# Optimization experiments

Measured on AMD Instinct MI355X. Metric: run time of the kernel, lower is better.

The kernel has to match this reference:

```python
import jax, jax.numpy as jnp
import numpy as np

B, F_NODES, E = 1024, 128, 1024   # graphs, nodes/graph, edges/graph
H, HEADS = 128, 4
HD = H // HEADS


def setup_inputs() -> dict:
    key = jax.random.key(0)
    ks = jax.random.split(key, 24)
    f32 = jnp.float32
    n = jax.random.normal
    d = {
        "x": n(ks[0], (B, F_NODES), f32),
        "edge_index": jax.random.randint(ks[1], (2, E), 0, F_NODES, dtype=jnp.int32),
        # input projection Linear(1, H)
        "w_in": n(ks[2], (1, H), f32) * 0.5,
        "b_in": n(ks[3], (H,), f32) * 0.02,
        # GAT layer 0: heads=4, concat=True, per-head dim HD
        "gat0_w": n(ks[4], (H, H), f32) * (1.0 / np.sqrt(H)),
        "gat0_as": n(ks[5], (HEADS, HD), f32) * 0.1,
        "gat0_ad": n(ks[6], (HEADS, HD), f32) * 0.1,
        "gat0_b": n(ks[7], (H,), f32) * 0.02,
        "bn0_g": 1.0 + 0.1 * n(ks[8], (H,), f32),
        "bn0_b": 0.1 * n(ks[9], (H,), f32),
        "bn0_m": 0.1 * n(ks[10], (H,), f32),
        "bn0_v": 1.0 + 0.1 * jax.random.uniform(ks[11], (H,), f32),
        # GAT layer 1: heads=1, concat=False
        "gat1_w": n(ks[12], (H, H), f32) * (1.0 / np.sqrt(H)),
        "gat1_as": n(ks[13], (1, H), f32) * 0.1,
        "gat1_ad": n(ks[14], (1, H), f32) * 0.1,
        "gat1_b": n(ks[15], (H,), f32) * 0.02,
        "bn1_g": 1.0 + 0.1 * n(ks[16], (H,), f32),
        "bn1_b": 0.1 * n(ks[17], (H,), f32),
        "bn1_m": 0.1 * n(ks[18], (H,), f32),
        "bn1_v": 1.0 + 0.1 * jax.random.uniform(ks[19], (H,), f32),
        # classifier MLP H -> H//2 -> 1
        "w1": n(ks[20], (H, H // 2), f32) * (1.0 / np.sqrt(H)),
        "b1": n(ks[21], (H // 2,), f32) * 0.02,
        "w2": n(ks[22], (H // 2, 1), f32) * (1.0 / np.sqrt(H // 2)),
        "b2": n(ks[23], (1,), f32) * 0.02,
    }
    return d


def _gat(h, src, dst, N, W, a_s, a_d, b, concat):
    # PyG GATConv (shared lin for src/dst, leaky_relu slope 0.2, softmax over dst)
    heads, hd = a_s.shape
    xh = (h @ W).reshape(N, heads, hd)                      # [N, heads, hd]
    e = jax.nn.leaky_relu(
        jnp.sum(xh * a_s[None], -1)[src] + jnp.sum(xh * a_d[None], -1)[dst],
        0.2,
    )                                                        # [Etot, heads]
    m = jax.ops.segment_max(e, dst, num_segments=N)
    ex = jnp.exp(e - m[dst])
    s = jax.ops.segment_sum(ex, dst, num_segments=N)
    alpha = ex / s[dst]
    out = jax.ops.segment_sum(xh[src] * alpha[..., None], dst, num_segments=N)
    out = out.reshape(N, heads * hd) if concat else out[:, 0]
    return out + b


def _bn(h, g, b, m, v):
    return (h - m) / jnp.sqrt(v + 1e-5) * g + b


def reference(x, edge_index, w_in, b_in,
              gat0_w, gat0_as, gat0_ad, gat0_b, bn0_g, bn0_b, bn0_m, bn0_v,
              gat1_w, gat1_as, gat1_ad, gat1_b, bn1_g, bn1_b, bn1_m, bn1_v,
              w1, b1, w2, b2):
    Bsz, Fn = x.shape
    N = Bsz * Fn
    h = jax.nn.relu(x.reshape(N, 1) @ w_in + b_in)           # [N, H]
    # replicate per-graph edges with node offsets, then add self loops
    offs = jnp.arange(Bsz, dtype=edge_index.dtype) * Fn
    eib = (edge_index[:, None, :] + offs[None, :, None]).reshape(2, -1)
    loops = jnp.arange(N, dtype=edge_index.dtype)
    src = jnp.concatenate([eib[0], loops])
    dst = jnp.concatenate([eib[1], loops])
    h = _gat(h, src, dst, N, gat0_w, gat0_as, gat0_ad, gat0_b, True)
    h = jax.nn.relu(_bn(h, bn0_g, bn0_b, bn0_m, bn0_v))
    h = _gat(h, src, dst, N, gat1_w, gat1_as, gat1_ad, gat1_b, False)
    h = jax.nn.relu(_bn(h, bn1_g, bn1_b, bn1_m, bn1_v))
    # global mean pool (each graph has exactly Fn nodes)
    hp = h.reshape(Bsz, Fn, -1).mean(axis=1)                 # [B, H]
    z = jax.nn.relu(hp @ w1 + b1)
    return z @ w2 + b2                                       # [B, 1]
```

## Files before the change

kernel.cpp:

```cpp
#include <hip/hip_runtime.h>

#define FN   128
#define HDIM 128
#define NH   4
#define HSZ  32
#define EB   1024
#define ET   1152
#define RSW  132

typedef __attribute__((ext_vector_type(8))) short bf16x8;
typedef __attribute__((ext_vector_type(4))) float f32x4;
typedef unsigned int u32;
typedef unsigned short u16;

union U8 { bf16x8 v; u32 u[4]; };

__device__ __forceinline__ u32 pack_hl(float v) {
  const u32 u = __float_as_uint(v);
  const u32 hib = u & 0xFFFF0000u;
  const float lo = v - __uint_as_float(hib);
  return hib | (__float_as_uint(lo) >> 16);
}
__device__ __forceinline__ float unpack_val(u32 p) {
  return __uint_as_float(p & 0xFFFF0000u) + __uint_as_float(p << 16);
}
__device__ __forceinline__ float lrelu(float v) {
  return (v > 0.f) ? v : 0.2f * v;
}

__device__ __forceinline__ void unpack_frag(const u32* __restrict__ q,
                                            bf16x8& hi, bf16x8& lo)
{
  const uint4 p0 = *(const uint4*)(q);
  const uint4 p1 = *(const uint4*)(q + 4);
  U8 H, L;
  H.u[0] = (p0.x >> 16) | (p0.y & 0xFFFF0000u);
  L.u[0] = (p0.x & 0xFFFFu) | (p0.y << 16);
  H.u[1] = (p0.z >> 16) | (p0.w & 0xFFFF0000u);
  L.u[1] = (p0.z & 0xFFFFu) | (p0.w << 16);
  H.u[2] = (p1.x >> 16) | (p1.y & 0xFFFF0000u);
  L.u[2] = (p1.x & 0xFFFFu) | (p1.y << 16);
  H.u[3] = (p1.z >> 16) | (p1.w & 0xFFFF0000u);
  L.u[3] = (p1.z & 0xFFFFu) | (p1.w << 16);
  hi = H.v; lo = L.v;
}

__global__ __launch_bounds__(256) void prep_w_kernel(
    const float* __restrict__ g0w, const float* __restrict__ g1w,
    u16* __restrict__ wf)
{
  const int idx = blockIdx.x * 256 + threadIdx.x;
  const int layer = idx >> 14;
  const int r = idx & 16383;
  const int c  = r >> 11;
  const int kc = (r >> 9) & 3;
  const int l  = (r >> 3) & 63;
  const int j  = r & 7;
  const int k = kc * 32 + (l >> 4) * 8 + j;
  const int n = c * 16 + (l & 15);
  const float* W = layer ? g1w : g0w;
  const float v = W[k * HDIM + n];
  const u32 u = __float_as_uint(v);
  const u32 hib = u & 0xFFFF0000u;
  const float lo = v - __uint_as_float(hib);
  wf[layer * 32768 + r]         = (u16)(u >> 16);
  wf[layer * 32768 + 16384 + r] = (u16)(__float_as_uint(lo) >> 16);
}

__global__ __launch_bounds__(256) void prep_csr_kernel(
    const int* __restrict__ ei, int* __restrict__ csr)
{
  __shared__ int deg[FN], rp[FN + 1], fill[FN];
  const int t = threadIdx.x;
  if (t < FN) { deg[t] = 0; fill[t] = 0; }
  __syncthreads();
  for (int e = t; e < EB; e += 256) atomicAdd(&deg[ei[EB + e]], 1);
  __syncthreads();
  if (t == 0) {
    int acc = 0;
    for (int n = 0; n < FN; ++n) { rp[n] = acc; acc += deg[n] + 1; }
    rp[FN] = acc;
  }
  __syncthreads();
  if (t < FN) {
    const int dn = deg[t];
    int rk = 0;
    for (int m = 0; m < FN; ++m) {
      const int dm = deg[m];
      rk += (dm > dn) || (dm == dn && m < t);
    }
    csr[ET + FN + 1 + rk] = t;
    csr[ET + t] = rp[t];
    if (t == 0) csr[ET + FN] = rp[FN];
  }
  __syncthreads();
  for (int e = t; e < EB; e += 256) {
    const int d = ei[EB + e], s = ei[e];
    const int p = rp[d] + atomicAdd(&fill[d], 1);
    csr[p] = s | (d << 8);
  }
  if (t < FN) csr[rp[t] + deg[t]] = t | (t << 8);
}

__device__ __forceinline__ void mfma_gemm_acc(const u32* __restrict__ F,
                                              const u16* __restrict__ wf,
                                              int lw, int lane, f32x4 acc[4][2])
{
  const int cg = lw & 3, rh = lw >> 2;
  const int m = lane & 15, quad = lane >> 4;

  #pragma unroll
  for (int s = 0; s < 4; ++s)
    #pragma unroll
    for (int ct = 0; ct < 2; ++ct) acc[s][ct] = (f32x4){0.f, 0.f, 0.f, 0.f};

  const u16* bbase = wf + (cg * 8) * 512 + lane * 8;

  #pragma unroll
  for (int kc = 0; kc < 4; ++kc) {
    bf16x8 bhi[2], blo[2];
    #pragma unroll
    for (int ct = 0; ct < 2; ++ct) {
      const u16* bp = bbase + ct * 2048 + kc * 512;
      bhi[ct] = *(const bf16x8*)bp;
      blo[ct] = *(const bf16x8*)(bp + 16384);
    }
    #pragma unroll
    for (int s = 0; s < 4; ++s) {
      const u32* ap = F + (rh * 64 + s * 16 + m) * RSW + quad * 8 + kc * 32;
      bf16x8 ahi, alo;
      unpack_frag(ap, ahi, alo);
      #pragma unroll
      for (int ct = 0; ct < 2; ++ct) {
        acc[s][ct] = __builtin_amdgcn_mfma_f32_16x16x32_bf16(ahi, bhi[ct], acc[s][ct], 0, 0, 0);
        acc[s][ct] = __builtin_amdgcn_mfma_f32_16x16x32_bf16(alo, bhi[ct], acc[s][ct], 0, 0, 0);
        acc[s][ct] = __builtin_amdgcn_mfma_f32_16x16x32_bf16(ahi, blo[ct], acc[s][ct], 0, 0, 0);
      }
    }
  }
}

__device__ __forceinline__ void store_acc(float* __restrict__ sg, int lw,
                                          int lane, const f32x4 acc[4][2])
{
  const int cg = lw & 3, rh = lw >> 2;
  const int m = lane & 15, quad = lane >> 4;
  #pragma unroll
  for (int s = 0; s < 4; ++s) {
    const int row0 = rh * 64 + s * 16 + quad * 4;
    #pragma unroll
    for (int ct = 0; ct < 2; ++ct)
      #pragma unroll
      for (int r = 0; r < 4; ++r)
        sg[(row0 + r) * RSW + cg * 32 + ct * 16 + m] = acc[s][ct][r];
  }
}

__global__ __launch_bounds__(512) void gnn_fused_kernel(
    const float* __restrict__ x,
    const float* __restrict__ w_in, const float* __restrict__ b_in,
    const float* __restrict__ g0as, const float* __restrict__ g0ad,
    const float* __restrict__ g0b,
    const float* __restrict__ bn0g, const float* __restrict__ bn0b,
    const float* __restrict__ bn0m, const float* __restrict__ bn0v,
    const float* __restrict__ g1as, const float* __restrict__ g1ad,
    const float* __restrict__ g1b,
    const float* __restrict__ bn1g, const float* __restrict__ bn1b,
    const float* __restrict__ bn1m, const float* __restrict__ bn1v,
    const float* __restrict__ w1, const float* __restrict__ b1,
    const float* __restrict__ w2, const float* __restrict__ b2,
    const u16* __restrict__ wf, const int* __restrict__ csr,
    float* __restrict__ out)
{
  __shared__ u32   F[FN * RSW];
  __shared__ int   s_src[ET];
  __shared__ int   s_rp[FN + 1];
  __shared__ int   s_perm[FN];
  __shared__ float s_scr[1280];
  __shared__ float s_bn[512];

  const int t = threadIdx.x;
  const int gid = blockIdx.x;
  const int lane = t & 63;
  const int lw = t >> 6;
  float* s_es = s_scr;
  float* s_ed = s_scr + 512;
  float* s_rs = s_scr + 1024;
  f32x4 acc[4][2];

  for (int e = t; e < ET; e += 512) s_src[e] = csr[e];
  if (t < FN + 1) s_rp[t] = csr[ET + t];
  if (t < FN)     s_perm[t] = csr[ET + FN + 1 + t];
  if (t < 256) {
    const int layer = t >> 7;
    const int col = t & 127;
    const float bb = layer ? g1b[col]  : g0b[col];
    const float bm = layer ? bn1m[col] : bn0m[col];
    const float bv = layer ? bn1v[col] : bn0v[col];
    const float bg = layer ? bn1g[col] : bn0g[col];
    const float bt = layer ? bn1b[col] : bn0b[col];
    const float q = bg * rsqrtf(bv + 1e-5f);
    s_bn[layer * 256 + col] = q;
    s_bn[layer * 256 + 128 + col] = (bb - bm) * q + bt;
  }
  {
    const int j = t & 127, q = t >> 7;
    const float wv = w_in[j], bv = b_in[j];
    const size_t xb = (size_t)gid * FN;
    for (int n = q * 32; n < q * 32 + 32; ++n) {
      const float v = fmaxf(fmaf(x[xb + n], wv, bv), 0.f);
      F[n * RSW + j] = pack_hl(v);
    }
  }
  __syncthreads();

  mfma_gemm_acc(F, wf, lw, lane, acc);
  __syncthreads();
  store_acc((float*)F, lw, lane, acc);
  __syncthreads();

  {
    const int hh = t >> 7, n = t & 127;
    const float* row = (const float*)F + n * RSW + hh * HSZ;
    float accs = 0.f, accd = 0.f;
    #pragma unroll
    for (int s = 0; s < 8; ++s) {
      const int d = ((n + s) & 7) * 4;
      const float4 v  = *(const float4*)(row + d);
      const float4 as = *(const float4*)(g0as + hh * HSZ + d);
      const float4 ad = *(const float4*)(g0ad + hh * HSZ + d);
      accs += v.x*as.x + v.y*as.y + v.z*as.z + v.w*as.w;
      accd += v.x*ad.x + v.y*ad.y + v.z*ad.z + v.w*ad.w;
    }
    s_es[hh * 128 + n] = accs;
    s_ed[hh * 128 + n] = accd;
  }
  __syncthreads();

  {
    const int slot = t & 127, hh = t >> 7;
    const int n = s_perm[slot];
    const int cb = hh * HSZ;
    const float* Ff = (const float*)F;
    const int e0 = s_rp[n], e1 = s_rp[n + 1];
    const float edv = s_ed[hh * 128 + n];
    const float* esb = s_es + hh * 128;
    float sum = 0.f;
    float4 a[8];
    #pragma unroll
    for (int i = 0; i < 8; ++i) a[i] = make_float4(0.f, 0.f, 0.f, 0.f);
    for (int e = e0; e < e1; ++e) {
      const int s = s_src[e] & 127;
      const float al = __expf(lrelu(esb[s] + edv));
      sum += al;
      const float* rp_ = Ff + s * RSW + cb;
      #pragma unroll
      for (int i = 0; i < 8; ++i) {
        const float4 vv = *(const float4*)(rp_ + i * 4);
        a[i].x = fmaf(al, vv.x, a[i].x); a[i].y = fmaf(al, vv.y, a[i].y);
        a[i].z = fmaf(al, vv.z, a[i].z); a[i].w = fmaf(al, vv.w, a[i].w);
      }
    }
    const float rsv = 1.f / sum;
    __syncthreads();
    #pragma unroll
    for (int i = 0; i < 8; ++i) {
      const int col = cb + i * 4;
      const float4 q = *(const float4*)&s_bn[col];
      const float4 r = *(const float4*)&s_bn[128 + col];
      uint4 p;
      p.x = pack_hl(fmaxf(fmaf(a[i].x * rsv, q.x, r.x), 0.f));
      p.y = pack_hl(fmaxf(fmaf(a[i].y * rsv, q.y, r.y), 0.f));
      p.z = pack_hl(fmaxf(fmaf(a[i].z * rsv, q.z, r.z), 0.f));
      p.w = pack_hl(fmaxf(fmaf(a[i].w * rsv, q.w, r.w), 0.f));
      *(uint4*)(F + n * RSW + col) = p;
    }
  }
  __syncthreads();

  mfma_gemm_acc(F, wf + 32768, lw, lane, acc);
  __syncthreads();
  store_acc((float*)F, lw, lane, acc);
  __syncthreads();

  {
    const int n = t >> 2, c = t & 3;
    const float* row = (const float*)F + n * RSW + c * 32;
    float accs = 0.f, accd = 0.f;
    #pragma unroll
    for (int i = 0; i < 8; ++i) {
      const int d = i * 4;
      const float4 v  = *(const float4*)(row + d);
      const float4 as = *(const float4*)(g1as + c * 32 + d);
      const float4 ad = *(const float4*)(g1ad + c * 32 + d);
      accs += v.x*as.x + v.y*as.y + v.z*as.z + v.w*as.w;
      accd += v.x*ad.x + v.y*ad.y + v.z*ad.z + v.w*ad.w;
    }
    s_es[t] = accs;
    s_ed[t] = accd;
  }
  __syncthreads();
  if (t < 128) {
    const float* pe = s_es + t * 4;
    const float* pd = s_ed + t * 4;
    s_rs[t]       = pe[0] + pe[1] + pe[2] + pe[3];
    s_rs[128 + t] = pd[0] + pd[1] + pd[2] + pd[3];
  }
  __syncthreads();

  {
    const int slot = t & 127, cg = t >> 7;
    const int n = s_perm[slot];
    const int cb = cg * HSZ;
    const float* Ff = (const float*)F;
    const int e0 = s_rp[n], e1 = s_rp[n + 1];
    const float edv = s_rs[128 + n];
    float sum = 0.f;
    float4 a[8];
    #pragma unroll
    for (int i = 0; i < 8; ++i) a[i] = make_float4(0.f, 0.f, 0.f, 0.f);
    for (int e = e0; e < e1; ++e) {
      const int s = s_src[e] & 127;
      const float al = __expf(lrelu(s_rs[s] + edv));
      sum += al;
      const float* rp_ = Ff + s * RSW + cb;
      #pragma unroll
      for (int i = 0; i < 8; ++i) {
        const float4 vv = *(const float4*)(rp_ + i * 4);
        a[i].x = fmaf(al, vv.x, a[i].x); a[i].y = fmaf(al, vv.y, a[i].y);
        a[i].z = fmaf(al, vv.z, a[i].z); a[i].w = fmaf(al, vv.w, a[i].w);
      }
    }
    const float rsv = 1.f / sum;
    __syncthreads();
    #pragma unroll
    for (int i = 0; i < 8; ++i) {
      const int col = cb + i * 4;
      const float4 q = *(const float4*)&s_bn[256 + col];
      const float4 r = *(const float4*)&s_bn[384 + col];
      uint4 p;
      p.x = __float_as_uint(fmaxf(fmaf(a[i].x * rsv, q.x, r.x), 0.f));
      p.y = __float_as_uint(fmaxf(fmaf(a[i].y * rsv, q.y, r.y), 0.f));
      p.z = __float_as_uint(fmaxf(fmaf(a[i].z * rsv, q.z, r.z), 0.f));
      p.w = __float_as_uint(fmaxf(fmaf(a[i].w * rsv, q.w, r.w), 0.f));
      *(uint4*)(F + n * RSW + col) = p;
    }
  }
  __syncthreads();

  {
    const int j = t & 127, q = t >> 7;
    float p = 0.f;
    for (int n = q * 32; n < q * 32 + 32; ++n)
      p += __uint_as_float(F[n * RSW + j]);
    s_es[q * 128 + j] = p;
  }
  __syncthreads();
  if (t < 128) {
    s_ed[t] = (s_es[t] + s_es[t + 128] + s_es[t + 256] + s_es[t + 384])
              * (1.f / 128.f);
  }
  __syncthreads();
  {
    const int j = t & 63, part = t >> 6;
    float a = 0.f;
    #pragma unroll
    for (int k = part * 16; k < part * 16 + 16; ++k)
      a = fmaf(s_ed[k], w1[k * 64 + j], a);
    s_es[part * 64 + j] = a;
  }
  __syncthreads();
  if (t < 64) {
    float a = b1[t];
    #pragma unroll
    for (int p = 0; p < 8; ++p) a += s_es[p * 64 + t];
    a = fmaxf(a, 0.f);
    float v = a * w2[t];
    #pragma unroll
    for (int off = 32; off > 0; off >>= 1) v += __shfl_down(v, off, 64);
    if (t == 0) out[gid] = v + b2[0];
  }
}

extern "C" void kernel_launch(void* const* d_in, const int* in_sizes, int n_in,
                              void* d_out, int out_size, void* d_ws, size_t ws_size,
                              hipStream_t stream)
{
  const float* x    = (const float*)d_in[0];
  const int*   ei   = (const int*)d_in[1];
  const float* w_in = (const float*)d_in[2];
  const float* b_in = (const float*)d_in[3];
  const float* g0w  = (const float*)d_in[4];
  const float* g0as = (const float*)d_in[5];
  const float* g0ad = (const float*)d_in[6];
  const float* g0b  = (const float*)d_in[7];
  const float* bn0g = (const float*)d_in[8];
  const float* bn0b = (const float*)d_in[9];
  const float* bn0m = (const float*)d_in[10];
  const float* bn0v = (const float*)d_in[11];
  const float* g1w  = (const float*)d_in[12];
  const float* g1as = (const float*)d_in[13];
  const float* g1ad = (const float*)d_in[14];
  const float* g1b  = (const float*)d_in[15];
  const float* bn1g = (const float*)d_in[16];
  const float* bn1b = (const float*)d_in[17];
  const float* bn1m = (const float*)d_in[18];
  const float* bn1v = (const float*)d_in[19];
  const float* w1   = (const float*)d_in[20];
  const float* b1   = (const float*)d_in[21];
  const float* w2   = (const float*)d_in[22];
  const float* b2   = (const float*)d_in[23];

  u16* wf  = (u16*)d_ws;
  int* csr = (int*)((char*)d_ws + 131072);

  prep_w_kernel<<<128, 256, 0, stream>>>(g0w, g1w, wf);
  prep_csr_kernel<<<1, 256, 0, stream>>>(ei, csr);
  gnn_fused_kernel<<<1024, 512, 0, stream>>>(x, w_in, b_in,
      g0as, g0ad, g0b, bn0g, bn0b, bn0m, bn0v,
      g1as, g1ad, g1b, bn1g, bn1b, bn1m, bn1v,
      w1, b1, w2, b2, wf, csr, (float*)d_out);
}
```

Baseline: 188.2 us.

## Merge prep kernels, shrink CSR to u16, unroll edge aggregation by two

```diff
diff --git a/kernel.cpp b/kernel.cpp
--- a/kernel.cpp
+++ b/kernel.cpp
@@ -20,9 +20,6 @@
   const u32 hib = u & 0xFFFF0000u;
   const float lo = v - __uint_as_float(hib);
   return hib | (__float_as_uint(lo) >> 16);
-}
-__device__ __forceinline__ float unpack_val(u32 p) {
-  return __uint_as_float(p & 0xFFFF0000u) + __uint_as_float(p << 16);
 }
 __device__ __forceinline__ float lrelu(float v) {
   return (v > 0.f) ? v : 0.2f * v;
@@ -45,10 +42,45 @@
   hi = H.v; lo = L.v;
 }
 
-__global__ __launch_bounds__(256) void prep_w_kernel(
+__global__ __launch_bounds__(256) void prep_kernel(
     const float* __restrict__ g0w, const float* __restrict__ g1w,
-    u16* __restrict__ wf)
-{
+    const int* __restrict__ ei,
+    u16* __restrict__ wf, u16* __restrict__ csrS, int* __restrict__ csrI)
+{
+  if (blockIdx.x == 128) {
+    __shared__ int deg[FN], rp[FN + 1], fill[FN];
+    const int t = threadIdx.x;
+    if (t < FN) { deg[t] = 0; fill[t] = 0; }
+    __syncthreads();
+    for (int e = t; e < EB; e += 256) atomicAdd(&deg[ei[EB + e]], 1);
+    __syncthreads();
+    if (t == 0) {
+      int acc = 0;
+      for (int n = 0; n < FN; ++n) { rp[n] = acc; acc += deg[n] + 1; }
+      rp[FN] = acc;
+    }
+    __syncthreads();
+    if (t < FN) {
+      const int dn = deg[t];
+      int rk = 0;
+      for (int m = 0; m < FN; ++m) {
+        const int dm = deg[m];
+        rk += (dm > dn) || (dm == dn && m < t);
+      }
+      csrI[129 + rk] = t;
+      csrI[t] = rp[t];
+      if (t == 0) csrI[FN] = rp[FN];
+    }
+    __syncthreads();
+    for (int e = t; e < EB; e += 256) {
+      const int d = ei[EB + e], s = ei[e];
+      const int p = rp[d] + atomicAdd(&fill[d], 1);
+      csrS[p] = (u16)s;
+    }
+    if (t < FN) csrS[rp[t] + deg[t]] = (u16)t;
+    return;
+  }
+
   const int idx = blockIdx.x * 256 + threadIdx.x;
   const int layer = idx >> 14;
   const int r = idx & 16383;
@@ -67,41 +99,6 @@
   wf[layer * 32768 + 16384 + r] = (u16)(__float_as_uint(lo) >> 16);
 }
 
-__global__ __launch_bounds__(256) void prep_csr_kernel(
-    const int* __restrict__ ei, int* __restrict__ csr)
-{
-  __shared__ int deg[FN], rp[FN + 1], fill[FN];
-  const int t = threadIdx.x;
-  if (t < FN) { deg[t] = 0; fill[t] = 0; }
-  __syncthreads();
-  for (int e = t; e < EB; e += 256) atomicAdd(&deg[ei[EB + e]], 1);
-  __syncthreads();
-  if (t == 0) {
-    int acc = 0;
-    for (int n = 0; n < FN; ++n) { rp[n] = acc; acc += deg[n] + 1; }
-    rp[FN] = acc;
-  }
-  __syncthreads();
-  if (t < FN) {
-    const int dn = deg[t];
-    int rk = 0;
-    for (int m = 0; m < FN; ++m) {
-      const int dm = deg[m];
-      rk += (dm > dn) || (dm == dn && m < t);
-    }
-    csr[ET + FN + 1 + rk] = t;
-    csr[ET + t] = rp[t];
-    if (t == 0) csr[ET + FN] = rp[FN];
-  }
-  __syncthreads();
-  for (int e = t; e < EB; e += 256) {
-    const int d = ei[EB + e], s = ei[e];
-    const int p = rp[d] + atomicAdd(&fill[d], 1);
-    csr[p] = s | (d << 8);
-  }
-  if (t < FN) csr[rp[t] + deg[t]] = t | (t << 8);
-}
-
 __device__ __forceinline__ void mfma_gemm_acc(const u32* __restrict__ F,
                                               const u16* __restrict__ wf,
                                               int lw, int lane, f32x4 acc[4][2])
@@ -156,7 +153,7 @@
   }
 }
 
-__global__ __launch_bounds__(512) void gnn_fused_kernel(
+__global__ __launch_bounds__(512, 4) void gnn_fused_kernel(
     const float* __restrict__ x,
     const float* __restrict__ w_in, const float* __restrict__ b_in,
     const float* __restrict__ g0as, const float* __restrict__ g0ad,
@@ -169,13 +166,14 @@
     const float* __restrict__ bn1m, const float* __restrict__ bn1v,
     const float* __restrict__ w1, const float* __restrict__ b1,
     const float* __restrict__ w2, const float* __restrict__ b2,
-    const u16* __restrict__ wf, const int* __restrict__ csr,
+    const u16* __restrict__ wf, const u16* __restrict__ csrS,
+    const int* __restrict__ csrI,
     float* __restrict__ out)
 {
   __shared__ u32   F[FN * RSW];
-  __shared__ int   s_src[ET];
   __shared__ int   s_rp[FN + 1];
   __shared__ int   s_perm[FN];
+  __shared__ u16   s_src[ET];
   __shared__ float s_scr[1280];
   __shared__ float s_bn[512];
 
@@ -188,11 +186,12 @@
   float* s_rs = s_scr + 1024;
   f32x4 acc[4][2];
 
-  for (int e = t; e < ET; e += 512) s_src[e] = csr[e];
-  if (t < FN + 1) s_rp[t] = csr[ET + t];
-  if (t < FN)     s_perm[t] = csr[ET + FN + 1 + t];
-  if (t < 256) {
-    const int layer = t >> 7;
+  for (int w = t; w < ET / 2; w += 512)
+    ((u32*)s_src)[w] = ((const u32*)csrS)[w];
+  if (t < FN + 1) s_rp[t] = csrI[t];
+  if (t < FN)     s_perm[t] = csrI[129 + t];
+  if (t >= 256 && t < 512) {
+    const int layer = (t >> 7) & 1;
     const int col = t & 127;
     const float bb = layer ? g1b[col]  : g0b[col];
     const float bm = layer ? bn1m[col] : bn0m[col];
@@ -249,11 +248,29 @@
     float4 a[8];
     #pragma unroll
     for (int i = 0; i < 8; ++i) a[i] = make_float4(0.f, 0.f, 0.f, 0.f);
-    for (int e = e0; e < e1; ++e) {
-      const int s = s_src[e] & 127;
-      const float al = __expf(lrelu(esb[s] + edv));
+    int e = e0;
+    for (; e + 1 < e1; e += 2) {
+      const int s0 = s_src[e], s1 = s_src[e + 1];
+      const float al0 = __expf(lrelu(esb[s0] + edv));
+      const float al1 = __expf(lrelu(esb[s1] + edv));
+      sum += al0 + al1;
+      const float* r0 = Ff + s0 * RSW + cb;
+      const float* r1 = Ff + s1 * RSW + cb;
+      #pragma unroll
+      for (int i = 0; i < 8; ++i) {
+        const float4 v0 = *(const float4*)(r0 + i * 4);
+        const float4 v1 = *(const float4*)(r1 + i * 4);
+        a[i].x = fmaf(al0, v0.x, fmaf(al1, v1.x, a[i].x));
+        a[i].y = fmaf(al0, v0.y, fmaf(al1, v1.y, a[i].y));
+        a[i].z = fmaf(al0, v0.z, fmaf(al1, v1.z, a[i].z));
+        a[i].w = fmaf(al0, v0.w, fmaf(al1, v1.w, a[i].w));
+      }
+    }
+    if (e < e1) {
+      const int s0 = s_src[e];
+      const float al = __expf(lrelu(esb[s0] + edv));
       sum += al;
-      const float* rp_ = Ff + s * RSW + cb;
+      const float* rp_ = Ff + s0 * RSW + cb;
       #pragma unroll
       for (int i = 0; i < 8; ++i) {
         const float4 vv = *(const float4*)(rp_ + i * 4);
@@ -319,11 +336,29 @@
     float4 a[8];
     #pragma unroll
     for (int i = 0; i < 8; ++i) a[i] = make_float4(0.f, 0.f, 0.f, 0.f);
-    for (int e = e0; e < e1; ++e) {
-      const int s = s_src[e] & 127;
-      const float al = __expf(lrelu(s_rs[s] + edv));
+    int e = e0;
+    for (; e + 1 < e1; e += 2) {
+      const int s0 = s_src[e], s1 = s_src[e + 1];
+      const float al0 = __expf(lrelu(s_rs[s0] + edv));
+      const float al1 = __expf(lrelu(s_rs[s1] + edv));
+      sum += al0 + al1;
+      const float* r0 = Ff + s0 * RSW + cb;
+      const float* r1 = Ff + s1 * RSW + cb;
+      #pragma unroll
+      for (int i = 0; i < 8; ++i) {
+        const float4 v0 = *(const float4*)(r0 + i * 4);
+        const float4 v1 = *(const float4*)(r1 + i * 4);
+        a[i].x = fmaf(al0, v0.x, fmaf(al1, v1.x, a[i].x));
+        a[i].y = fmaf(al0, v0.y, fmaf(al1, v1.y, a[i].y));
+        a[i].z = fmaf(al0, v0.z, fmaf(al1, v1.z, a[i].z));
+        a[i].w = fmaf(al0, v0.w, fmaf(al1, v1.w, a[i].w));
+      }
+    }
+    if (e < e1) {
+      const int s0 = s_src[e];
+      const float al = __expf(lrelu(s_rs[s0] + edv));
       sum += al;
-      const float* rp_ = Ff + s * RSW + cb;
+      const float* rp_ = Ff + s0 * RSW + cb;
       #pragma unroll
       for (int i = 0; i < 8; ++i) {
         const float4 vv = *(const float4*)(rp_ + i * 4);
@@ -411,13 +446,13 @@
   const float* w2   = (const float*)d_in[22];
   const float* b2   = (const float*)d_in[23];
 
-  u16* wf  = (u16*)d_ws;
-  int* csr = (int*)((char*)d_ws + 131072);
-
-  prep_w_kernel<<<128, 256, 0, stream>>>(g0w, g1w, wf);
-  prep_csr_kernel<<<1, 256, 0, stream>>>(ei, csr);
+  u16* wf   = (u16*)d_ws;
+  u16* csrS = (u16*)((char*)d_ws + 131072);
+  int* csrI = (int*)((char*)d_ws + 131072 + 2304);
+
+  prep_kernel<<<129, 256, 0, stream>>>(g0w, g1w, ei, wf, csrS, csrI);
   gnn_fused_kernel<<<1024, 512, 0, stream>>>(x, w_in, b_in,
       g0as, g0ad, g0b, bn0g, bn0b, bn0m, bn0v,
       g1as, g1ad, g1b, bn1g, bn1b, bn1m, bn1v,
-      w1, b1, w2, b2, wf, csr, (float*)d_out);
-}
+      w1, b1, w2, b2, wf, csrS, csrI, (float*)d_out);
+}
```

New measurement: 186.3 us. About the same (-1.0%).
